# Optimization experiments

Hardware: AMD Instinct MI355X
Metric: run time of the kernel (lower is better)

The kernel has to match this reference:

```python
import jax, jax.numpy as jnp
import numpy as np

NUM_HEADS = 16

def setup_inputs() -> dict:
    key = jax.random.key(0)
    k1, k2, k3 = jax.random.split(key, 3)
    B, S, D = 2, 2048, 1024
    x = jax.random.normal(k1, (B, S, D), dtype=jnp.float32)
    Wqkv = jax.random.normal(k2, (D, 3 * D), dtype=jnp.float32) * (1.0 / np.sqrt(D))
    bqkv = jnp.zeros((3 * D,), dtype=jnp.float32)
    Wo = jax.random.normal(k3, (D, D), dtype=jnp.float32) * (1.0 / np.sqrt(D))
    bo = jnp.zeros((D,), dtype=jnp.float32)
    return {"x": x, "Wqkv": Wqkv, "bqkv": bqkv, "Wo": Wo, "bo": bo}

def reference(x, Wqkv, bqkv, Wo, bo):
    B, S, D = x.shape
    H = NUM_HEADS
    hd = D // H
    # qkv projection, split into per-head q, k, v: [B, H, S, hd]
    qkv = (x @ Wqkv + bqkv).reshape(B, S, H, 3 * hd).transpose(0, 2, 1, 3)
    q, k, v = jnp.split(qkv, 3, axis=-1)
    # causal attention scores [B, H, S, S]
    scores = jnp.einsum('bhqd,bhkd->bhqk', q, k)
    causal = jnp.tril(jnp.ones((S, S), dtype=bool))  # True = keep
    scores = jnp.where(causal, scores, -jnp.inf)
    attn = jax.nn.softmax(scores / np.sqrt(hd).astype(np.float32), axis=-1)
    # dropout is identity in eval mode
    ctx = jnp.einsum('bhqk,bhkd->bhqd', attn, v)  # [B, H, S, hd]
    ctx = ctx.transpose(0, 2, 1, 3).reshape(B, S, D)
    return ctx @ Wo + bo
```

## Files before the change

kernel.cpp:

```cpp
#include <hip/hip_runtime.h>


typedef __attribute__((ext_vector_type(8))) __bf16 bf16x8;
typedef __attribute__((ext_vector_type(4))) float f32x4;
typedef __attribute__((ext_vector_type(4))) short short4v;

__device__ __forceinline__ unsigned short f2bf(float f) {
    union { float f; unsigned u; } v; v.f = f;
    unsigned r = v.u + 0x7fffu + ((v.u >> 16) & 1u);
    return (unsigned short)(r >> 16);
}

__device__ __forceinline__ unsigned pack_bf16x2_trunc(float a, float b) {
#if defined(__HIP_DEVICE_COMPILE__)
    return __builtin_amdgcn_perm(__builtin_bit_cast(unsigned, a),
                                 __builtin_bit_cast(unsigned, b), 0x03020706u);
#else
    return 0u;
#endif
}

__device__ __forceinline__ float fast_exp2(float x) {
#if defined(__HIP_DEVICE_COMPILE__)
    return __builtin_amdgcn_exp2f(x);
#else
    return x;
#endif
}

__device__ __forceinline__ void async_copy16(const unsigned short* g, unsigned short* l) {
    __builtin_amdgcn_global_load_lds(
        (const __attribute__((address_space(1))) unsigned int*)g,
        (__attribute__((address_space(3))) unsigned int*)l, 16, 0, 0);
}

__device__ __forceinline__ f32x4 mfma16x16x16(short4v a, short4v b, f32x4 c) {
#if defined(__HIP_DEVICE_COMPILE__)
    return __builtin_amdgcn_mfma_f32_16x16x16bf16_1k(a, b, c, 0, 0, 0);
#else
    return c;
#endif
}

__global__ __launch_bounds__(256) void convert_f32_bf16(
    const float* __restrict__ in, unsigned short* __restrict__ out)
{
    size_t i = ((size_t)blockIdx.x * 256 + threadIdx.x) * 8;
    float4 v0 = *(const float4*)(in + i);
    float4 v1 = *(const float4*)(in + i + 4);
    ushort4 a, b;
    a.x = f2bf(v0.x); a.y = f2bf(v0.y); a.z = f2bf(v0.z); a.w = f2bf(v0.w);
    b.x = f2bf(v1.x); b.y = f2bf(v1.y); b.z = f2bf(v1.z); b.w = f2bf(v1.w);
    *(ushort4*)(out + i) = a;
    *(ushort4*)(out + i + 4) = b;
}

__global__ __launch_bounds__(256) void transpose_f32_bf16(
    const float* __restrict__ in, unsigned short* __restrict__ out, int K, int N)
{
    __shared__ float T[64][65];
    const int tid = threadIdx.x;
    const int n0 = blockIdx.x * 64, k0 = blockIdx.y * 64;
#pragma unroll
    for (int i = 0; i < 4; i++) {
        int idx = tid + i * 256;
        int r = idx >> 4, c4 = (idx & 15) * 4;
        float4 v = *(const float4*)(in + (size_t)(k0 + r) * N + n0 + c4);
        T[r][c4 + 0] = v.x; T[r][c4 + 1] = v.y; T[r][c4 + 2] = v.z; T[r][c4 + 3] = v.w;
    }
    __syncthreads();
#pragma unroll
    for (int i = 0; i < 4; i++) {
        int idx = tid + i * 256;
        int n = idx >> 4, k4 = (idx & 15) * 4;
        ushort4 o;
        o.x = f2bf(T[k4 + 0][n]); o.y = f2bf(T[k4 + 1][n]);
        o.z = f2bf(T[k4 + 2][n]); o.w = f2bf(T[k4 + 3][n]);
        *(ushort4*)(out + (size_t)(n0 + n) * K + k0 + k4) = o;
    }
}

__global__ __launch_bounds__(256) void transpose_v(
    const unsigned short* __restrict__ vrow, unsigned short* __restrict__ vt)
{
    __shared__ unsigned short T[64 * 72];
    const int tid = threadIdx.x;
    const int bh = blockIdx.y;
    const int s0 = blockIdx.x * 64;
    const unsigned short* src = vrow + ((size_t)bh * 2048 + s0) * 64;
    unsigned short* dst = vt + (size_t)bh * 64 * 2048 + s0;
#pragma unroll
    for (int i = 0; i < 2; i++) {
        int idx = tid + i * 256;
        int s = idx >> 3, dg = (idx & 7) * 8;
        *(uint4*)&T[s * 72 + dg] = *(const uint4*)(src + s * 64 + dg);
    }
    __syncthreads();
#pragma unroll
    for (int i = 0; i < 2; i++) {
        int idx = tid + i * 256;
        int d = idx >> 3, sg = (idx & 7) * 8;
        ushort4 a, b;
        a.x = T[(sg + 0) * 72 + d]; a.y = T[(sg + 1) * 72 + d];
        a.z = T[(sg + 2) * 72 + d]; a.w = T[(sg + 3) * 72 + d];
        b.x = T[(sg + 4) * 72 + d]; b.y = T[(sg + 5) * 72 + d];
        b.z = T[(sg + 6) * 72 + d]; b.w = T[(sg + 7) * 72 + d];
        *(ushort4*)(dst + (size_t)d * 2048 + sg) = a;
        *(ushort4*)(dst + (size_t)d * 2048 + sg + 4) = b;
    }
}

__global__ __launch_bounds__(256) void gemm_qkv_bf(
    const unsigned short* __restrict__ Xbf,
    const unsigned short* __restrict__ WT,
    const float* __restrict__ bias,
    unsigned short* __restrict__ qws, unsigned short* __restrict__ kws,
    unsigned short* __restrict__ vrow)
{
    const int K = 1024;
    __shared__ __align__(16) unsigned short smem[128 * 136];
    unsigned short* As = smem;
    unsigned short* Bs = smem + 8192;
    const int tid = threadIdx.x;
    const int m0 = blockIdx.y * 128, n0 = blockIdx.x * 128;
    const int wave = tid >> 6, lane = tid & 63;
    const int wm = (wave >> 1) * 64, wn = (wave & 1) * 64;
    const int quad = lane >> 4, l16 = lane & 15;
    const int lrow = lane >> 3, lgrp = lane & 7;
    const int sg = lgrp ^ lrow;

    f32x4 acc[4][4];
    const f32x4 Z4 = {0.f, 0.f, 0.f, 0.f};
#pragma unroll
    for (int i = 0; i < 4; i++)
#pragma unroll
        for (int j = 0; j < 4; j++) acc[i][j] = Z4;

    for (int k0 = 0; k0 < K; k0 += 64) {
        __syncthreads();
#pragma unroll
        for (int c = 0; c < 4; c++) {
            int nb = (wave * 4 + c) * 8;
            async_copy16(Xbf + (size_t)(m0 + nb + lrow) * K + k0 + sg * 8, &As[nb * 64]);
            async_copy16(WT  + (size_t)(n0 + nb + lrow) * K + k0 + sg * 8, &Bs[nb * 64]);
        }
        __syncthreads();
#pragma unroll
        for (int kk = 0; kk < 2; kk++) {
            int pg = ((kk * 4 + quad) ^ (l16 & 7)) * 8;
            bf16x8 af[4], bfr[4];
#pragma unroll
            for (int mi = 0; mi < 4; mi++) af[mi] = *(const bf16x8*)&As[(wm + mi * 16 + l16) * 64 + pg];
#pragma unroll
            for (int ni = 0; ni < 4; ni++) bfr[ni] = *(const bf16x8*)&Bs[(wn + ni * 16 + l16) * 64 + pg];
#pragma unroll
            for (int mi = 0; mi < 4; mi++)
#pragma unroll
                for (int ni = 0; ni < 4; ni++)
                    acc[mi][ni] = __builtin_amdgcn_mfma_f32_16x16x32_bf16(af[mi], bfr[ni], acc[mi][ni], 0, 0, 0);
        }
    }
    __syncthreads();
#pragma unroll
    for (int ni = 0; ni < 4; ni++) {
        int colL = wn + ni * 16 + l16;
        int col = n0 + colL;
        int t = (col % 192) >> 6;
        float bv = bias[col];
        float scl = (t == 1) ? 0.18033688f : 1.0f;
#pragma unroll
        for (int mi = 0; mi < 4; mi++)
#pragma unroll
            for (int r = 0; r < 4; r++) {
                int row = wm + mi * 16 + quad * 4 + r;
                smem[row * 136 + colL] = f2bf((acc[mi][ni][r] + bv) * scl);
            }
    }
    __syncthreads();
#pragma unroll
    for (int i = 0; i < 8; i++) {
        int idx = tid + i * 256;
        int row = idx >> 4, g = idx & 15;
        int colL = g * 8;
        uint4 w = *(const uint4*)&smem[row * 136 + colL];
        int col = n0 + colL;
        int h = col / 192, rem = col % 192, t = rem >> 6, d = rem & 63;
        int grow = m0 + row;
        int b = grow >> 11, s = grow & 2047;
        unsigned short* dst = (t == 0) ? qws : (t == 1) ? kws : vrow;
        *(uint4*)(dst + ((size_t)(b * 16 + h) * 2048 + s) * 64 + d) = w;
    }
}

__global__ __launch_bounds__(128) void attn(
    const unsigned short* __restrict__ qws, const unsigned short* __restrict__ kws,
    const unsigned short* __restrict__ vtws, unsigned short* __restrict__ ctx)
{
    __shared__ __align__(16) unsigned short Qs[64 * 64];
    __shared__ __align__(16) unsigned short Ks[64 * 64];
    __shared__ __align__(16) unsigned short Vt[64][72];

    const int tid = threadIdx.x;
    const int wave = tid >> 6, lane = tid & 63, quad = lane >> 4, l16 = lane & 15;
    const int lrow = lane >> 3, lgrp = lane & 7;
    const int sg = lgrp ^ lrow;

    const int i = blockIdx.x;
    const int tile = 31 - (i >> 5);
    const int bh = i & 31;
    const int q0 = tile * 64;

    const unsigned short* Q  = qws + (size_t)bh * 2048 * 64;
    const unsigned short* Kp = kws + (size_t)bh * 2048 * 64;
    const unsigned short* Vp = vtws + (size_t)bh * 64 * 2048;

#pragma unroll
    for (int c = 0; c < 4; c++) {
        int rb = (wave * 4 + c) * 8;
        async_copy16(Q + (size_t)(q0 + rb + lrow) * 64 + sg * 8, &Qs[rb * 64]);
    }

    const int wq = wave * 32;
    f32x4 o[4][2];
    const f32x4 Z4 = {0.f, 0.f, 0.f, 0.f};
#pragma unroll
    for (int dt = 0; dt < 4; dt++)
#pragma unroll
        for (int qt = 0; qt < 2; qt++) o[dt][qt] = Z4;
    float lsum[2] = {0.f, 0.f};

    const int jmax = tile + 1;
    for (int j = 0; j < jmax; j++) {
        const int kb0 = j * 64;
        __syncthreads();
#pragma unroll
        for (int c = 0; c < 4; c++) {
            int rb = (wave * 4 + c) * 8;
            async_copy16(Kp + (size_t)(kb0 + rb + lrow) * 64 + sg * 8, &Ks[rb * 64]);
        }
#pragma unroll
        for (int ii = 0; ii < 4; ii++) {
            int id2 = tid + ii * 128;
            int row = id2 >> 3, c = (id2 & 7) * 8;
            *(uint4*)&Vt[row][c] = *(const uint4*)(Vp + (size_t)row * 2048 + kb0 + c);
        }
        __syncthreads();

        if (kb0 <= q0 + wq + 31) {
            f32x4 sc[4][2];
#pragma unroll
            for (int kt = 0; kt < 4; kt++)
#pragma unroll
                for (int qt = 0; qt < 2; qt++) sc[kt][qt] = Z4;
#pragma unroll
            for (int kk = 0; kk < 2; kk++) {
                int pg = ((kk * 4 + quad) ^ (l16 & 7)) * 8;
                bf16x8 ak[4], bq[2];
#pragma unroll
                for (int kt = 0; kt < 4; kt++) ak[kt] = *(const bf16x8*)&Ks[(kt * 16 + l16) * 64 + pg];
#pragma unroll
                for (int qt = 0; qt < 2; qt++) bq[qt] = *(const bf16x8*)&Qs[(wq + qt * 16 + l16) * 64 + pg];
#pragma unroll
                for (int kt = 0; kt < 4; kt++)
#pragma unroll
                    for (int qt = 0; qt < 2; qt++)
                        sc[kt][qt] = __builtin_amdgcn_mfma_f32_16x16x32_bf16(ak[kt], bq[qt], sc[kt][qt], 0, 0, 0);
            }
            short4v pb[4][2];
            if (kb0 + 63 <= q0 + wq) {
#pragma unroll
                for (int qt = 0; qt < 2; qt++)
#pragma unroll
                    for (int kt = 0; kt < 4; kt++) {
                        float p0 = fast_exp2(sc[kt][qt][0]);
                        float p1 = fast_exp2(sc[kt][qt][1]);
                        float p2 = fast_exp2(sc[kt][qt][2]);
                        float p3 = fast_exp2(sc[kt][qt][3]);
                        lsum[qt] += (p0 + p1) + (p2 + p3);
                        uint2 uu;
                        uu.x = pack_bf16x2_trunc(p0, p1);
                        uu.y = pack_bf16x2_trunc(p2, p3);
                        pb[kt][qt] = __builtin_bit_cast(short4v, uu);
                    }
            } else {
#pragma unroll
                for (int qt = 0; qt < 2; qt++) {
                    int qg = q0 + wq + qt * 16 + l16;
#pragma unroll
                    for (int kt = 0; kt < 4; kt++) {
                        float p[4];
#pragma unroll
                        for (int r = 0; r < 4; r++) {
                            int key = kb0 + kt * 16 + quad * 4 + r;
                            float t = fast_exp2(sc[kt][qt][r]);
                            p[r] = (key <= qg) ? t : 0.f;
                        }
                        lsum[qt] += (p[0] + p[1]) + (p[2] + p[3]);
                        uint2 uu;
                        uu.x = pack_bf16x2_trunc(p[0], p[1]);
                        uu.y = pack_bf16x2_trunc(p[2], p[3]);
                        pb[kt][qt] = __builtin_bit_cast(short4v, uu);
                    }
                }
            }
#pragma unroll
            for (int kt = 0; kt < 4; kt++) {
#pragma unroll
                for (int dt = 0; dt < 4; dt++) {
                    short4v av = *(const short4v*)&Vt[dt * 16 + l16][kt * 16 + quad * 4];
#pragma unroll
                    for (int qt = 0; qt < 2; qt++)
                        o[dt][qt] = mfma16x16x16(av, pb[kt][qt], o[dt][qt]);
                }
            }
        }
    }
#pragma unroll
    for (int qt = 0; qt < 2; qt++) {
        lsum[qt] += __shfl_xor(lsum[qt], 16);
        lsum[qt] += __shfl_xor(lsum[qt], 32);
    }
    const int b = bh >> 4, h = bh & 15;
#pragma unroll
    for (int qt = 0; qt < 2; qt++) {
        int qg = q0 + wq + qt * 16 + l16;
        float inv = 1.0f / lsum[qt];
#pragma unroll
        for (int dt = 0; dt < 4; dt++) {
            ushort4 ov;
            ov.x = f2bf(o[dt][qt][0] * inv);
            ov.y = f2bf(o[dt][qt][1] * inv);
            ov.z = f2bf(o[dt][qt][2] * inv);
            ov.w = f2bf(o[dt][qt][3] * inv);
            *(ushort4*)(ctx + (size_t)(b * 2048 + qg) * 1024 + h * 64 + dt * 16 + quad * 4) = ov;
        }
    }
}

__global__ __launch_bounds__(256) void gemm_out(
    const unsigned short* __restrict__ Ctx, const unsigned short* __restrict__ WT,
    const float* __restrict__ bias, float* __restrict__ Out)
{
    const int K = 1024, N = 1024;
    __shared__ __align__(16) unsigned short As[64 * 64];
    __shared__ __align__(16) unsigned short Bs[128 * 64];
    const int tid = threadIdx.x;
    const int m0 = blockIdx.y * 64, n0 = blockIdx.x * 128;
    const int wave = tid >> 6, lane = tid & 63;
    const int wm = (wave >> 1) * 32, wn = (wave & 1) * 64;
    const int quad = lane >> 4, l16 = lane & 15;
    const int lrow = lane >> 3, lgrp = lane & 7;
    const int sg = lgrp ^ lrow;

    f32x4 acc[2][4];
    const f32x4 Z4 = {0.f, 0.f, 0.f, 0.f};
#pragma unroll
    for (int i = 0; i < 2; i++)
#pragma unroll
        for (int j = 0; j < 4; j++) acc[i][j] = Z4;

    for (int k0 = 0; k0 < K; k0 += 64) {
        __syncthreads();
#pragma unroll
        for (int c = 0; c < 2; c++) {
            int nb = (wave * 2 + c) * 8;
            async_copy16(Ctx + (size_t)(m0 + nb + lrow) * K + k0 + sg * 8, &As[nb * 64]);
        }
#pragma unroll
        for (int c = 0; c < 4; c++) {
            int nb = (wave * 4 + c) * 8;
            async_copy16(WT + (size_t)(n0 + nb + lrow) * K + k0 + sg * 8, &Bs[nb * 64]);
        }
        __syncthreads();
#pragma unroll
        for (int kk = 0; kk < 2; kk++) {
            int pg = ((kk * 4 + quad) ^ (l16 & 7)) * 8;
            bf16x8 af[2], bfr[4];
#pragma unroll
            for (int mi = 0; mi < 2; mi++) af[mi] = *(const bf16x8*)&As[(wm + mi * 16 + l16) * 64 + pg];
#pragma unroll
            for (int ni = 0; ni < 4; ni++) bfr[ni] = *(const bf16x8*)&Bs[(wn + ni * 16 + l16) * 64 + pg];
#pragma unroll
            for (int mi = 0; mi < 2; mi++)
#pragma unroll
                for (int ni = 0; ni < 4; ni++)
                    acc[mi][ni] = __builtin_amdgcn_mfma_f32_16x16x32_bf16(af[mi], bfr[ni], acc[mi][ni], 0, 0, 0);
        }
    }
#pragma unroll
    for (int mi = 0; mi < 2; mi++)
#pragma unroll
        for (int ni = 0; ni < 4; ni++) {
            int col = n0 + wn + ni * 16 + l16;
            float bv = bias[col];
#pragma unroll
            for (int r = 0; r < 4; r++) {
                int row = m0 + wm + mi * 16 + quad * 4 + r;
                Out[(size_t)row * N + col] = acc[mi][ni][r] + bv;
            }
        }
}

extern "C" void kernel_launch(void* const* d_in, const int* in_sizes, int n_in,
                              void* d_out, int out_size, void* d_ws, size_t ws_size,
                              hipStream_t stream) {
    const float* x    = (const float*)d_in[0];
    const float* Wqkv = (const float*)d_in[1];
    const float* bqkv = (const float*)d_in[2];
    const float* Wo   = (const float*)d_in[3];
    const float* bo   = (const float*)d_in[4];
    float* out = (float*)d_out;

    const size_t R = 4194304;
    unsigned short* q    = (unsigned short*)d_ws;
    unsigned short* k    = q + R;
    unsigned short* vrow = k + R;
    unsigned short* ctx  = vrow + R;
    unsigned short* xbf  = ctx + R;
    unsigned short* vt   = xbf;
    unsigned short* wqkvT = ctx;
    unsigned short* woT   = q;

    convert_f32_bf16<<<dim3(2048), 256, 0, stream>>>(x, xbf);
    transpose_f32_bf16<<<dim3(48, 16), 256, 0, stream>>>(Wqkv, wqkvT, 1024, 3072);
    gemm_qkv_bf<<<dim3(24, 32), 256, 0, stream>>>(xbf, wqkvT, bqkv, q, k, vrow);
    transpose_v<<<dim3(32, 32), 256, 0, stream>>>(vrow, vt);
    attn<<<dim3(1024), 128, 0, stream>>>(q, k, vt, ctx);
    transpose_f32_bf16<<<dim3(16, 16), 256, 0, stream>>>(Wo, woT, 1024, 1024);
    gemm_out<<<dim3(8, 64), 256, 0, stream>>>(ctx, woT, bo, out);
}
```

Before: 200.6 us.

## Split long causal attention tiles across two blocks and combine partials

Query tiles 17-31 now have their key range split into two chunks handled by separate blocks, scheduled through a constant job table with the longest jobs first. Each chunk writes its unnormalized output in bf16 plus its row sums to a workspace, and a new combine kernel adds the two and normalizes. The goal is to balance the causal triangle's uneven work across more blocks and cut the tail. The cost is an extra launch, extra global traffic, and some bf16 rounding of the partials. This relies on the softmax using a fixed scale with no running max.

```diff
diff --git a/kernel.cpp b/kernel.cpp
--- a/kernel.cpp
+++ b/kernel.cpp
@@ -192,9 +192,24 @@
     }
 }
 
+__device__ __constant__ unsigned ATTN_JOBS[47] = {
+    16u | (0u<<8) | (17u<<16),
+    15u | (0u<<8) | (16u<<16), 30u | (0u<<8) | (16u<<16), 31u | (0u<<8) | (16u<<16), 31u | (16u<<8) | (32u<<16),
+    14u | (0u<<8) | (15u<<16), 28u | (0u<<8) | (15u<<16), 29u | (0u<<8) | (15u<<16), 29u | (15u<<8) | (30u<<16), 30u | (16u<<8) | (31u<<16),
+    13u | (0u<<8) | (14u<<16), 26u | (0u<<8) | (14u<<16), 27u | (0u<<8) | (14u<<16), 27u | (14u<<8) | (28u<<16), 28u | (15u<<8) | (29u<<16),
+    12u | (0u<<8) | (13u<<16), 24u | (0u<<8) | (13u<<16), 25u | (0u<<8) | (13u<<16), 25u | (13u<<8) | (26u<<16), 26u | (14u<<8) | (27u<<16),
+    11u | (0u<<8) | (12u<<16), 22u | (0u<<8) | (12u<<16), 23u | (0u<<8) | (12u<<16), 23u | (12u<<8) | (24u<<16), 24u | (13u<<8) | (25u<<16),
+    10u | (0u<<8) | (11u<<16), 20u | (0u<<8) | (11u<<16), 21u | (0u<<8) | (11u<<16), 21u | (11u<<8) | (22u<<16), 22u | (12u<<8) | (23u<<16),
+     9u | (0u<<8) | (10u<<16), 18u | (0u<<8) | (10u<<16), 19u | (0u<<8) | (10u<<16), 19u | (10u<<8) | (20u<<16), 20u | (11u<<8) | (21u<<16),
+     8u | (0u<<8) | ( 9u<<16), 17u | (0u<<8) | ( 9u<<16), 17u | ( 9u<<8) | (18u<<16), 18u | (10u<<8) | (19u<<16),
+     7u | (0u<<8) | ( 8u<<16),  6u | (0u<<8) | ( 7u<<16),  5u | (0u<<8) | ( 6u<<16),  4u | (0u<<8) | ( 5u<<16),
+     3u | (0u<<8) | ( 4u<<16),  2u | (0u<<8) | ( 3u<<16),  1u | (0u<<8) | ( 2u<<16),  0u | (0u<<8) | ( 1u<<16),
+};
+
 __global__ __launch_bounds__(128) void attn(
     const unsigned short* __restrict__ qws, const unsigned short* __restrict__ kws,
-    const unsigned short* __restrict__ vtws, unsigned short* __restrict__ ctx)
+    const unsigned short* __restrict__ vtws, unsigned short* __restrict__ ctx,
+    unsigned short* __restrict__ Opart, float* __restrict__ lpart)
 {
     __shared__ __align__(16) unsigned short Qs[64 * 64];
     __shared__ __align__(16) unsigned short Ks[64 * 64];
@@ -205,10 +220,12 @@
     const int lrow = lane >> 3, lgrp = lane & 7;
     const int sg = lgrp ^ lrow;
 
-    const int i = blockIdx.x;
-    const int tile = 31 - (i >> 5);
-    const int bh = i & 31;
+    const unsigned job = ATTN_JOBS[blockIdx.x >> 5];
+    const int bh = blockIdx.x & 31;
+    const int tile = job & 0xff;
+    const int js = (job >> 8) & 0xff, je = (job >> 16) & 0xff;
     const int q0 = tile * 64;
+    const bool split = tile >= 17;
 
     const unsigned short* Q  = qws + (size_t)bh * 2048 * 64;
     const unsigned short* Kp = kws + (size_t)bh * 2048 * 64;
@@ -229,8 +246,7 @@
         for (int qt = 0; qt < 2; qt++) o[dt][qt] = Z4;
     float lsum[2] = {0.f, 0.f};
 
-    const int jmax = tile + 1;
-    for (int j = 0; j < jmax; j++) {
+    for (int j = js; j < je; j++) {
         const int kb0 = j * 64;
         __syncthreads();
 #pragma unroll
@@ -320,20 +336,69 @@
         lsum[qt] += __shfl_xor(lsum[qt], 16);
         lsum[qt] += __shfl_xor(lsum[qt], 32);
     }
+    if (!split) {
+        const int b = bh >> 4, h = bh & 15;
+#pragma unroll
+        for (int qt = 0; qt < 2; qt++) {
+            int qg = q0 + wq + qt * 16 + l16;
+            float inv = 1.0f / lsum[qt];
+#pragma unroll
+            for (int dt = 0; dt < 4; dt++) {
+                ushort4 ov;
+                ov.x = f2bf(o[dt][qt][0] * inv);
+                ov.y = f2bf(o[dt][qt][1] * inv);
+                ov.z = f2bf(o[dt][qt][2] * inv);
+                ov.w = f2bf(o[dt][qt][3] * inv);
+                *(ushort4*)(ctx + (size_t)(b * 2048 + qg) * 1024 + h * 64 + dt * 16 + quad * 4) = ov;
+            }
+        }
+    } else {
+        const int chunk = (js > 0) ? 1 : 0;
+        const size_t slot = (size_t)bh * 30 + (tile - 17) * 2 + chunk;
+        unsigned short* ob = Opart + slot * 4096;
+#pragma unroll
+        for (int qt = 0; qt < 2; qt++) {
+            int rl = wq + qt * 16 + l16;
+#pragma unroll
+            for (int dt = 0; dt < 4; dt++) {
+                ushort4 ov;
+                ov.x = f2bf(o[dt][qt][0]);
+                ov.y = f2bf(o[dt][qt][1]);
+                ov.z = f2bf(o[dt][qt][2]);
+                ov.w = f2bf(o[dt][qt][3]);
+                *(ushort4*)(ob + (size_t)rl * 64 + dt * 16 + quad * 4) = ov;
+            }
+            if (quad == 0) lpart[slot * 64 + rl] = lsum[qt];
+        }
+    }
+}
+
+__global__ __launch_bounds__(256) void attn_combine(
+    const unsigned short* __restrict__ Opart, const float* __restrict__ lpart,
+    unsigned short* __restrict__ ctx)
+{
+    const int t = 17 + blockIdx.x;
+    const int bh = blockIdx.y;
+    const int tid = threadIdx.x;
+    const int row = tid >> 2, dg = (tid & 3) * 16;
+    const size_t s0 = (size_t)bh * 30 + (t - 17) * 2;
+    const float inv = 1.0f / (lpart[s0 * 64 + row] + lpart[(s0 + 1) * 64 + row]);
+    const unsigned short* p1 = Opart + s0 * 4096 + (size_t)row * 64 + dg;
+    const unsigned short* p2 = p1 + 4096;
     const int b = bh >> 4, h = bh & 15;
-#pragma unroll
-    for (int qt = 0; qt < 2; qt++) {
-        int qg = q0 + wq + qt * 16 + l16;
-        float inv = 1.0f / lsum[qt];
-#pragma unroll
-        for (int dt = 0; dt < 4; dt++) {
-            ushort4 ov;
-            ov.x = f2bf(o[dt][qt][0] * inv);
-            ov.y = f2bf(o[dt][qt][1] * inv);
-            ov.z = f2bf(o[dt][qt][2] * inv);
-            ov.w = f2bf(o[dt][qt][3] * inv);
-            *(ushort4*)(ctx + (size_t)(b * 2048 + qg) * 1024 + h * 64 + dt * 16 + quad * 4) = ov;
-        }
+    unsigned short* dst = ctx + ((size_t)(b * 2048 + t * 64 + row)) * 1024 + h * 64 + dg;
+#pragma unroll
+    for (int g = 0; g < 2; g++) {
+        ushort a1[8], a2[8], ov[8];
+        *(uint4*)a1 = *(const uint4*)(p1 + g * 8);
+        *(uint4*)a2 = *(const uint4*)(p2 + g * 8);
+#pragma unroll
+        for (int e = 0; e < 8; e++) {
+            float f1 = __builtin_bit_cast(float, (unsigned)a1[e] << 16);
+            float f2 = __builtin_bit_cast(float, (unsigned)a2[e] << 16);
+            ov[e] = f2bf((f1 + f2) * inv);
+        }
+        *(uint4*)(dst + g * 8) = *(const uint4*)ov;
     }
 }
 
@@ -420,12 +485,15 @@
     unsigned short* vt   = xbf;
     unsigned short* wqkvT = ctx;
     unsigned short* woT   = q;
+    unsigned short* Opart = vrow;
+    float* lpart = (float*)(vrow + 960 * (size_t)4096);
 
     convert_f32_bf16<<<dim3(2048), 256, 0, stream>>>(x, xbf);
     transpose_f32_bf16<<<dim3(48, 16), 256, 0, stream>>>(Wqkv, wqkvT, 1024, 3072);
     gemm_qkv_bf<<<dim3(24, 32), 256, 0, stream>>>(xbf, wqkvT, bqkv, q, k, vrow);
     transpose_v<<<dim3(32, 32), 256, 0, stream>>>(vrow, vt);
-    attn<<<dim3(1024), 128, 0, stream>>>(q, k, vt, ctx);
+    attn<<<dim3(1504), 128, 0, stream>>>(q, k, vt, ctx, Opart, lpart);
+    attn_combine<<<dim3(15, 32), 256, 0, stream>>>(Opart, lpart, ctx);
     transpose_f32_bf16<<<dim3(16, 16), 256, 0, stream>>>(Wo, woT, 1024, 1024);
     gemm_out<<<dim3(8, 64), 256, 0, stream>>>(ctx, woT, bo, out);
 }
```

New measurement: 197.4 us. About the same (-1.6%).
